# Kernel tuning notes

Hardware: AMD Instinct MI355X
Metric: run time of the kernel (lower is better)

Reference implementation:

```python
import jax, jax.numpy as jnp
import numpy as np

_EPS = 1e-6

def _qmul(q1, q2):  # xyzw quaternion product
    x1, y1, z1, w1 = q1[..., 0], q1[..., 1], q1[..., 2], q1[..., 3]
    x2, y2, z2, w2 = q2[..., 0], q2[..., 1], q2[..., 2], q2[..., 3]
    return jnp.stack([
        w1 * x2 + x1 * w2 + y1 * z2 - z1 * y2,
        w1 * y2 + y1 * w2 + z1 * x2 - x1 * z2,
        w1 * z2 + z1 * w2 + x1 * y2 - y1 * x2,
        w1 * w2 - x1 * x2 - y1 * y2 - z1 * z2], axis=-1)

def _qrot(q, v):  # rotate v by unit quaternion q (xyzw)
    qv, qw = q[..., :3], q[..., 3:4]
    t = 2.0 * jnp.cross(qv, v)
    return v + qw * t + jnp.cross(qv, t)

def _so3_log(q):  # quaternion (xyzw) -> rotation vector phi
    qv, qw = q[..., :3], q[..., 3:4]
    n2 = jnp.sum(qv * qv, axis=-1, keepdims=True)
    small = n2 < _EPS * _EPS
    n = jnp.sqrt(jnp.where(small, 1.0, n2))
    factor = jnp.where(small,
                       2.0 / qw - (2.0 / 3.0) * n2 / qw ** 3,
                       2.0 * jnp.arctan2(n, qw) / n)
    return factor * qv

def _so3_exp(phi):  # rotation vector -> quaternion (xyzw)
    t2 = jnp.sum(phi * phi, axis=-1, keepdims=True)
    small = t2 < _EPS * _EPS
    theta = jnp.sqrt(jnp.where(small, 1.0, t2))
    half = 0.5 * theta
    s = jnp.where(small, 0.5 - t2 / 48.0, jnp.sin(half) / theta)
    w = jnp.where(small, 1.0 - t2 / 8.0, jnp.cos(half))
    return jnp.concatenate([s * phi, w], axis=-1)

def _jl(phi, v):  # SO3 left Jacobian J_l(phi) @ v
    t2 = jnp.sum(phi * phi, axis=-1, keepdims=True)
    small = t2 < _EPS * _EPS
    t2s = jnp.where(small, 1.0, t2)
    theta = jnp.sqrt(t2s)
    a = jnp.where(small, 0.5 - t2 / 24.0, (1.0 - jnp.cos(theta)) / t2s)
    b = jnp.where(small, 1.0 / 6.0 - t2 / 120.0, (theta - jnp.sin(theta)) / (t2s * theta))
    c1 = jnp.cross(phi, v)
    return v + a * c1 + b * jnp.cross(phi, c1)

def _jl_inv(phi, v):  # SO3 left Jacobian inverse J_l^{-1}(phi) @ v
    t2 = jnp.sum(phi * phi, axis=-1, keepdims=True)
    small = t2 < _EPS * _EPS
    t2s = jnp.where(small, 1.0, t2)
    theta = jnp.sqrt(t2s)
    s = jnp.sin(theta)
    s_safe = jnp.where(jnp.abs(s) < _EPS, _EPS, s)
    c = jnp.where(small, 1.0 / 12.0 + t2 / 720.0,
                  1.0 / t2s - (1.0 + jnp.cos(theta)) / (2.0 * theta * s_safe))
    c1 = jnp.cross(phi, v)
    return v - 0.5 * c1 + c * jnp.cross(phi, c1)

def _se3_inv(T):
    t, q = T[..., :3], T[..., 3:]
    qi = q * jnp.array([-1.0, -1.0, -1.0, 1.0], dtype=T.dtype)
    return jnp.concatenate([-_qrot(qi, t), qi], axis=-1)

def _se3_mul(T1, T2):
    t1, q1 = T1[..., :3], T1[..., 3:]
    t2, q2 = T2[..., :3], T2[..., 3:]
    return jnp.concatenate([t1 + _qrot(q1, t2), _qmul(q1, q2)], axis=-1)

def _se3_log(T):  # SE3 -> se3 [tau, phi]
    t, q = T[..., :3], T[..., 3:]
    phi = _so3_log(q)
    return jnp.concatenate([_jl_inv(phi, t), phi], axis=-1)

def _se3_exp(xi):  # se3 [tau, phi] -> SE3
    tau, phi = xi[..., :3], xi[..., 3:]
    q = _so3_exp(phi)
    return jnp.concatenate([_jl(phi, tau), q], axis=-1)

def _forward(input_poses, time):
    # duplicate first/last pose (inter_begin_and_end=True)
    poses = jnp.concatenate([input_poses[:, :1], input_poses, input_poses[:, -1:]], axis=1)
    B, P = poses.shape[0], poses.shape[1]
    S = P - 3  # number of spline segments
    u = time.reshape(-1)  # [K]
    K = u.shape[0]
    U = jnp.stack([jnp.ones_like(u), u, u * u, u * u * u], axis=0)  # [4,K]
    M = jnp.array([[5., 3., -3., 1.], [1., 3., 3., -2.], [0., 0., 0., 1.]], dtype=u.dtype) / 6.0
    w = M @ U  # [3,K] cumulative B-spline weights
    p0, p1 = poses[:, 0:S], poses[:, 1:S + 1]
    p2, p3 = poses[:, 2:S + 2], poses[:, 3:S + 3]
    d0 = _se3_log(_se3_mul(_se3_inv(p0), p1))  # [B,S,6]
    d1 = _se3_log(_se3_mul(_se3_inv(p1), p2))
    d2 = _se3_log(_se3_mul(_se3_inv(p2), p3))
    A0 = _se3_exp(d0[:, :, None, :] * w[0][None, None, :, None])  # [B,S,K,7]
    A1 = _se3_exp(d1[:, :, None, :] * w[1][None, None, :, None])
    A2 = _se3_exp(d2[:, :, None, :] * w[2][None, None, :, None])
    Td = jnp.broadcast_to(p0[:, :, None, :], (B, S, K, 7))
    out = _se3_mul(_se3_mul(_se3_mul(Td, A0), A1), A2)
    return out.reshape(B, S * K, 7)

def setup_inputs() -> dict:
    key = jax.random.key(0)
    k1, k2, k3 = jax.random.split(key, 3)
    B, N, K = 32, 2048, 32
    t = jax.random.normal(k1, (B, N, 3), dtype=jnp.float32) * 2.0
    q = jax.random.normal(k2, (B, N, 4), dtype=jnp.float32)
    q = q / jnp.linalg.norm(q, axis=-1, keepdims=True)
    q = jnp.where(q[..., 3:4] < 0, -q, q)  # qw >= 0 for well-conditioned Log
    input_poses = jnp.concatenate([t, q], axis=-1)
    time = jax.random.uniform(k3, (1, 1, K), dtype=jnp.float32)
    return {"input_poses": input_poses, "time": time}

def reference(input_poses, time):
    return _forward(input_poses, time)
```

## Files before the change

### kernel.cpp

```cpp
#include <hip/hip_runtime.h>
#include <cmath>

namespace {

typedef float f2 __attribute__((ext_vector_type(2)));

constexpr int BATCH  = 32;
constexpr int NPOSE  = 2048;
constexpr int KSAMP  = 32;
constexpr int NSEG   = NPOSE - 1;
constexpr int NDELTA = NPOSE + 1;
constexpr int SEGB   = 32;
constexpr int RSTRIDE = 6;
constexpr float EPS  = 1e-6f;
constexpr float EPS2 = 1e-12f;
constexpr float INV_TWO_PI = 0.15915494309189535f;

struct V3 { float x, y, z; };
struct Q4 { float x, y, z, w; };

__device__ __forceinline__ float frcp(float x)  { return __builtin_amdgcn_rcpf(x); }
__device__ __forceinline__ float fsqrt(float x) { return __builtin_amdgcn_sqrtf(x); }
__device__ __forceinline__ float fsin(float x)  { return __builtin_amdgcn_sinf(x * INV_TWO_PI); }
__device__ __forceinline__ float fcos(float x)  { return __builtin_amdgcn_cosf(x * INV_TWO_PI); }

__device__ __forceinline__ V3 v3add(V3 a, V3 b) { return {a.x + b.x, a.y + b.y, a.z + b.z}; }
__device__ __forceinline__ V3 v3sub(V3 a, V3 b) { return {a.x - b.x, a.y - b.y, a.z - b.z}; }
__device__ __forceinline__ V3 v3scl(V3 a, float s) { return {a.x * s, a.y * s, a.z * s}; }
__device__ __forceinline__ float v3dot(V3 a, V3 b) { return a.x * b.x + a.y * b.y + a.z * b.z; }
__device__ __forceinline__ V3 v3cross(V3 a, V3 b) {
    return {a.y * b.z - a.z * b.y, a.z * b.x - a.x * b.z, a.x * b.y - a.y * b.x};
}

__device__ __forceinline__ V3 qrot(Q4 q, V3 v) {
    V3 qv{q.x, q.y, q.z};
    V3 t = v3scl(v3cross(qv, v), 2.0f);
    return v3add(v3add(v, v3scl(t, q.w)), v3cross(qv, t));
}

__device__ __forceinline__ Q4 qmul(Q4 a, Q4 b) {
    return {a.w * b.x + a.x * b.w + a.y * b.z - a.z * b.y,
            a.w * b.y + a.y * b.w + a.z * b.x - a.x * b.z,
            a.w * b.z + a.z * b.w + a.x * b.y - a.y * b.x,
            a.w * b.w - a.x * b.x - a.y * b.y - a.z * b.z};
}

__device__ __forceinline__ float facos(float x) {
    float ax = fabsf(x);
    float p = -0.0012624911f;
    p = p * ax + 0.0066700901f;
    p = p * ax - 0.0170881256f;
    p = p * ax + 0.0308918810f;
    p = p * ax - 0.0501743046f;
    p = p * ax + 0.0889789874f;
    p = p * ax - 0.2145988016f;
    p = p * ax + 1.5707963050f;
    float r = fsqrt(fmaxf(1.0f - ax, 0.0f)) * p;
    return (x >= 0.0f) ? r : (3.14159265358979f - r);
}

__device__ __forceinline__ V3 so3_log(Q4 q) {
    V3 qv{q.x, q.y, q.z};
    float n2 = v3dot(qv, qv);
    bool small = n2 < EPS2;
    float n = fsqrt(small ? 1.0f : n2);
    float iw = frcp(q.w);
    float f_small = 2.0f * iw - (2.0f / 3.0f) * n2 * iw * iw * iw;
    float wc = fminf(fmaxf(q.w, -1.0f), 1.0f);
    float f_big = 2.0f * facos(wc) * frcp(n);
    return v3scl(qv, small ? f_small : f_big);
}

__device__ __forceinline__ V3 jl_inv(V3 phi, V3 v) {
    float t2 = v3dot(phi, phi);
    bool small = t2 < EPS2;
    float t2s = small ? 1.0f : t2;
    float theta = fsqrt(t2s);
    float s = fsin(theta), cth = fcos(theta);
    float s_safe = (fabsf(s) < EPS) ? EPS : s;
    float c_big = frcp(t2s) - (1.0f + cth) * frcp(2.0f * theta * s_safe);
    float c = small ? (1.0f / 12.0f + t2 * (1.0f / 720.0f)) : c_big;
    V3 c1 = v3cross(phi, v);
    return v3add(v3sub(v, v3scl(c1, 0.5f)), v3scl(v3cross(phi, c1), c));
}

struct V3p { f2 x, y, z; };
struct Q4p { f2 x, y, z, w; };
struct SE3p { V3p t; Q4p q; };

__device__ __forceinline__ f2 splat(float a) { return f2{a, a}; }

__device__ __forceinline__ SE3p se3_mul_p(const SE3p& A, const SE3p& B) {
    f2 cx = A.q.y * B.t.z - A.q.z * B.t.y;
    f2 cy = A.q.z * B.t.x - A.q.x * B.t.z;
    f2 cz = A.q.x * B.t.y - A.q.y * B.t.x;
    cx = cx + cx; cy = cy + cy; cz = cz + cz;
    SE3p r;
    r.t.x = A.t.x + B.t.x + A.q.w * cx + (A.q.y * cz - A.q.z * cy);
    r.t.y = A.t.y + B.t.y + A.q.w * cy + (A.q.z * cx - A.q.x * cz);
    r.t.z = A.t.z + B.t.z + A.q.w * cz + (A.q.x * cy - A.q.y * cx);
    r.q.x = A.q.w * B.q.x + A.q.x * B.q.w + A.q.y * B.q.z - A.q.z * B.q.y;
    r.q.y = A.q.w * B.q.y + A.q.y * B.q.w + A.q.z * B.q.x - A.q.x * B.q.z;
    r.q.z = A.q.w * B.q.z + A.q.z * B.q.w + A.q.x * B.q.y - A.q.y * B.q.x;
    r.q.w = A.q.w * B.q.w - A.q.x * B.q.x - A.q.y * B.q.y - A.q.z * B.q.z;
    return r;
}

__device__ __forceinline__ SE3p build_E(const float4& A, const float4& U,
                                        const float4& C1, const float4& C2,
                                        float wa, float wb) {
    const float inv_n = U.w;
    float tha = wa * A.w, thb = wb * A.w;
    float sa = fsin(0.5f * tha), ca = fcos(0.5f * tha);
    float sb = fsin(0.5f * thb), cb = fcos(0.5f * thb);
    float cAa = 2.0f * sa * sa * inv_n;
    float cAb = 2.0f * sb * sb * inv_n;
    float cBa = (tha - 2.0f * sa * ca) * inv_n;
    float cBb = (thb - 2.0f * sb * cb) * inv_n;
    f2 s2{sa, sb}, c2{ca, cb};
    f2 cA{cAa, cAb}, cB{cBa, cBb}, wh{wa, wb};
    SE3p E;
    E.q.x = s2 * splat(U.x); E.q.y = s2 * splat(U.y); E.q.z = s2 * splat(U.z);
    E.q.w = c2;
    E.t.x = wh * splat(A.x) + cA * splat(C1.x) + cB * splat(C2.x);
    E.t.y = wh * splat(A.y) + cA * splat(C1.y) + cB * splat(C2.y);
    E.t.z = wh * splat(A.z) + cA * splat(C1.z) + cB * splat(C2.z);
    return E;
}

__global__ __launch_bounds__(256) void lie_spline_fused(
    const float* __restrict__ poses,
    const float* __restrict__ timev,
    float* __restrict__ out)
{
    __shared__ float4 sdel[(SEGB + 2) * RSTRIDE];
    __shared__ __align__(16) float stage[SEGB * KSAMP * 7];

    const int b   = blockIdx.y;
    const int s0  = blockIdx.x * SEGB;
    const int tid = threadIdx.x;

    const int segl = tid >> 3;
    const int m    = tid & 7;
    const int s    = s0 + segl;

    const float4 uvec = reinterpret_cast<const float4*>(timev)[m];

    if (tid < SEGB + 2) {
        int i = min(s0 + tid, NDELTA - 1);
        int ia = max(i - 1, 0);
        int ib = min(i, NPOSE - 1);
        const float* Pa = poses + ((size_t)b * NPOSE + ia) * 7;
        const float* Pb = poses + ((size_t)b * NPOSE + ib) * 7;
        V3 ta{Pa[0], Pa[1], Pa[2]}; Q4 qa{Pa[3], Pa[4], Pa[5], Pa[6]};
        V3 tb{Pb[0], Pb[1], Pb[2]}; Q4 qb{Pb[3], Pb[4], Pb[5], Pb[6]};

        Q4 qi{-qa.x, -qa.y, -qa.z, qa.w};
        V3 trel = qrot(qi, v3sub(tb, ta));
        Q4 qrel = qmul(qi, qb);
        V3 phi = so3_log(qrel);
        V3 tau = jl_inv(phi, trel);

        float nphi = fsqrt(v3dot(phi, phi));
        float inv_n = frcp(fmaxf(nphi, 1e-20f));
        V3 u  = v3scl(phi, inv_n);
        V3 c1 = v3cross(u, tau);
        V3 c2 = v3cross(u, c1);

        float4* r = sdel + tid * RSTRIDE;
        r[0] = make_float4(tau.x, tau.y, tau.z, nphi);
        r[1] = make_float4(u.x,  u.y,  u.z,  inv_n);
        r[2] = make_float4(c1.x, c1.y, c1.z, 0.0f);
        r[3] = make_float4(c2.x, c2.y, c2.z, 0.0f);
        r[4] = make_float4(ta.x, ta.y, ta.z, qa.x);
        r[5] = make_float4(qa.y, qa.z, qa.w, 0.0f);
    }
    __syncthreads();

    if (s < NSEG) {
        const float4* R = sdel + segl * RSTRIDE;
        const float4 A0 = R[0],             U0 = R[1],               C10 = R[2],               C20 = R[3];
        const float4 P03 = R[4],            P46 = R[5];
        const float4 A1 = R[RSTRIDE],       U1 = R[RSTRIDE + 1],     C11 = R[RSTRIDE + 2],     C21 = R[RSTRIDE + 3];
        const float4 A2 = R[2 * RSTRIDE],   U2 = R[2 * RSTRIDE + 1], C12 = R[2 * RSTRIDE + 2], C22 = R[2 * RSTRIDE + 3];

        SE3p Tph;
        Tph.t.x = splat(P03.x); Tph.t.y = splat(P03.y); Tph.t.z = splat(P03.z);
        Tph.q.x = splat(P03.w); Tph.q.y = splat(P46.x); Tph.q.z = splat(P46.y);
        Tph.q.w = splat(P46.z);

        const float c6 = 1.0f / 6.0f;
        #define CHAIN(ua_, ub_, Tdst_)                                           \
        {                                                                        \
            float ua = (ua_), ub = (ub_);                                        \
            float ua2 = ua * ua, ua3 = ua2 * ua;                                 \
            float ub2 = ub * ub, ub3 = ub2 * ub;                                 \
            float w0a = (5.0f + 3.0f * ua - 3.0f * ua2 + ua3) * c6;              \
            float w0b = (5.0f + 3.0f * ub - 3.0f * ub2 + ub3) * c6;              \
            float w1a = (1.0f + 3.0f * ua + 3.0f * ua2 - 2.0f * ua3) * c6;       \
            float w1b = (1.0f + 3.0f * ub + 3.0f * ub2 - 2.0f * ub3) * c6;       \
            float w2a = ua3 * c6, w2b = ub3 * c6;                                \
            SE3p T = se3_mul_p(Tph, build_E(A0, U0, C10, C20, w0a, w0b));        \
            T = se3_mul_p(T, build_E(A1, U1, C11, C21, w1a, w1b));               \
            T = se3_mul_p(T, build_E(A2, U2, C12, C22, w2a, w2b));               \
            Tdst_ = T;                                                           \
        }

        float* sb_ = stage + segl * (KSAMP * 7) + m * 28;
        float4* sv = reinterpret_cast<float4*>(sb_);
        float2* s2v = reinterpret_cast<float2*>(sb_);

        {
            SE3p TA;
            CHAIN(uvec.x, uvec.y, TA)
            sv[0]  = make_float4(TA.t.x[0], TA.t.y[0], TA.t.z[0], TA.q.x[0]);
            sv[1]  = make_float4(TA.q.y[0], TA.q.z[0], TA.q.w[0], TA.t.x[1]);
            sv[2]  = make_float4(TA.t.y[1], TA.t.z[1], TA.q.x[1], TA.q.y[1]);
            s2v[6] = make_float2(TA.q.z[1], TA.q.w[1]);
        }
        {
            SE3p TB;
            CHAIN(uvec.z, uvec.w, TB)
            s2v[7] = make_float2(TB.t.x[0], TB.t.y[0]);
            sv[4]  = make_float4(TB.t.z[0], TB.q.x[0], TB.q.y[0], TB.q.z[0]);
            sv[5]  = make_float4(TB.q.w[0], TB.t.x[1], TB.t.y[1], TB.t.z[1]);
            sv[6]  = make_float4(TB.q.x[1], TB.q.y[1], TB.q.z[1], TB.q.w[1]);
        }
        #undef CHAIN
    }
    __syncthreads();

    int nseg_blk = min(NSEG - s0, SEGB);
    int nvec = nseg_blk * (KSAMP * 7 / 4);
    const float4* svv = reinterpret_cast<const float4*>(stage);
    float4* ov = reinterpret_cast<float4*>(out + ((size_t)b * NSEG + s0) * (size_t)(KSAMP * 7));
    for (int j = tid; j < nvec; j += 256) ov[j] = svv[j];
}

}

extern "C" void kernel_launch(void* const* d_in, const int* in_sizes, int n_in,
                              void* d_out, int out_size, void* d_ws, size_t ws_size,
                              hipStream_t stream) {
    const float* poses = (const float*)d_in[0];
    const float* timev = (const float*)d_in[1];
    float* out = (float*)d_out;
    (void)in_sizes; (void)n_in; (void)out_size; (void)d_ws; (void)ws_size;

    dim3 grid((NSEG + SEGB - 1) / SEGB, BATCH);
    lie_spline_fused<<<grid, 256, 0, stream>>>(poses, timev, out);
}
```

Baseline: 78.40 us.

## Split block tile into independent per-wave tiles to drop block barriers

Each 64-lane wave now owns its own 8-segment tile, with a private slice of the delta table and the output staging buffer in shared memory. Both __syncthreads calls are removed, so waves compute deltas, evaluate the spline and copy their results to global memory without waiting on each other. In exchange, each wave recomputes its two boundary deltas, so more poses are processed redundantly. Correctness also depends on LDS writes and reads inside one wavefront staying ordered without an explicit barrier.

After: 80.08 us. 1.02x slower.

```diff
diff --git a/kernel.cpp b/kernel.cpp
--- a/kernel.cpp
+++ b/kernel.cpp
@@ -10,7 +10,9 @@
 constexpr int KSAMP  = 32;
 constexpr int NSEG   = NPOSE - 1;
 constexpr int NDELTA = NPOSE + 1;
-constexpr int SEGB   = 32;
+constexpr int SEGW   = 8;
+constexpr int WAVES  = 4;
+constexpr int SEGB   = SEGW * WAVES;
 constexpr int RSTRIDE = 6;
 constexpr float EPS  = 1e-6f;
 constexpr float EPS2 = 1e-12f;
@@ -133,21 +135,21 @@
     const float* __restrict__ timev,
     float* __restrict__ out)
 {
-    __shared__ float4 sdel[(SEGB + 2) * RSTRIDE];
-    __shared__ __align__(16) float stage[SEGB * KSAMP * 7];
-
-    const int b   = blockIdx.y;
-    const int s0  = blockIdx.x * SEGB;
-    const int tid = threadIdx.x;
-
-    const int segl = tid >> 3;
-    const int m    = tid & 7;
-    const int s    = s0 + segl;
+    __shared__ float4 sdel[WAVES][(SEGW + 2) * RSTRIDE];
+    __shared__ __align__(16) float stage[WAVES][SEGW * KSAMP * 7];
+
+    const int b    = blockIdx.y;
+    const int tid  = threadIdx.x;
+    const int wid  = tid >> 6;
+    const int lane = tid & 63;
+    const int sW   = blockIdx.x * SEGB + wid * SEGW;
+    const int segl = lane >> 3;
+    const int m    = lane & 7;
 
     const float4 uvec = reinterpret_cast<const float4*>(timev)[m];
 
-    if (tid < SEGB + 2) {
-        int i = min(s0 + tid, NDELTA - 1);
+    if (lane < SEGW + 2) {
+        int i = min(sW + lane, NDELTA - 1);
         int ia = max(i - 1, 0);
         int ib = min(i, NPOSE - 1);
         const float* Pa = poses + ((size_t)b * NPOSE + ia) * 7;
@@ -167,7 +169,7 @@
         V3 c1 = v3cross(u, tau);
         V3 c2 = v3cross(u, c1);
 
-        float4* r = sdel + tid * RSTRIDE;
+        float4* r = sdel[wid] + lane * RSTRIDE;
         r[0] = make_float4(tau.x, tau.y, tau.z, nphi);
         r[1] = make_float4(u.x,  u.y,  u.z,  inv_n);
         r[2] = make_float4(c1.x, c1.y, c1.z, 0.0f);
@@ -175,10 +177,9 @@
         r[4] = make_float4(ta.x, ta.y, ta.z, qa.x);
         r[5] = make_float4(qa.y, qa.z, qa.w, 0.0f);
     }
-    __syncthreads();
-
-    if (s < NSEG) {
-        const float4* R = sdel + segl * RSTRIDE;
+
+    {
+        const float4* R = sdel[wid] + segl * RSTRIDE;
         const float4 A0 = R[0],             U0 = R[1],               C10 = R[2],               C20 = R[3];
         const float4 P03 = R[4],            P46 = R[5];
         const float4 A1 = R[RSTRIDE],       U1 = R[RSTRIDE + 1],     C11 = R[RSTRIDE + 2],     C21 = R[RSTRIDE + 3];
@@ -206,7 +207,7 @@
             Tdst_ = T;                                                           \
         }
 
-        float* sb_ = stage + segl * (KSAMP * 7) + m * 28;
+        float* sb_ = stage[wid] + segl * (KSAMP * 7) + m * 28;
         float4* sv = reinterpret_cast<float4*>(sb_);
         float2* s2v = reinterpret_cast<float2*>(sb_);
 
@@ -228,13 +229,14 @@
         }
         #undef CHAIN
     }
-    __syncthreads();
-
-    int nseg_blk = min(NSEG - s0, SEGB);
-    int nvec = nseg_blk * (KSAMP * 7 / 4);
-    const float4* svv = reinterpret_cast<const float4*>(stage);
-    float4* ov = reinterpret_cast<float4*>(out + ((size_t)b * NSEG + s0) * (size_t)(KSAMP * 7));
-    for (int j = tid; j < nvec; j += 256) ov[j] = svv[j];
+
+    {
+        int nseg_w = min(NSEG - sW, SEGW);
+        int nvec = nseg_w * (KSAMP * 7 / 4);
+        const float4* svv = reinterpret_cast<const float4*>(stage[wid]);
+        float4* ov = reinterpret_cast<float4*>(out + ((size_t)b * NSEG + sW) * (size_t)(KSAMP * 7));
+        for (int j = lane; j < nvec; j += 64) ov[j] = svv[j];
+    }
 }
 
 }
```
